# Optimization experiments

Hardware: AMD Instinct MI355X
Metric: run time of the kernel (lower is better)

## Reference

```python
import jax, jax.numpy as jnp
import numpy as np

N_NODES = 50000
N_EDGES = 800000
IN_FEAT = 512
OUT_FEAT = 128


def multispike(x):
    return jnp.floor(jnp.clip(4.0 * x, 0.0, 4.0) + 0.5) / 4.0


def setup_inputs() -> dict:
    key = jax.random.key(0)
    k1, k2, k3, k4, k5 = jax.random.split(key, 5)
    feat = jax.random.normal(k1, (N_NODES, IN_FEAT), dtype=jnp.float32)
    # Xavier-uniform-like init for the weight parameter
    limit = np.sqrt(6.0 / (IN_FEAT + OUT_FEAT)).astype(np.float32)
    weight = jax.random.uniform(k2, (IN_FEAT, OUT_FEAT), dtype=jnp.float32,
                                minval=-limit, maxval=limit)
    rows = jnp.sort(jax.random.randint(k3, (N_EDGES,), 0, N_NODES, dtype=jnp.int32))
    cols = jax.random.randint(k4, (N_EDGES,), 0, N_NODES, dtype=jnp.int32)
    edge_weight = jax.random.uniform(k5, (N_EDGES,), dtype=jnp.float32)
    return {"feat": feat, "weight": weight, "rows": rows, "cols": cols,
            "edge_weight": edge_weight}


def reference(feat, weight, rows, cols, edge_weight):
    # x = feat @ W                     [N, out_feat]
    x = jnp.matmul(feat, weight)
    # x = spmm(adj, x): out[i] = sum_{e: rows[e]==i} w_e * x[cols[e]]
    edge_feats = edge_weight[:, None] * x[cols]          # [E, out_feat]
    x = jax.ops.segment_sum(edge_feats, rows, num_segments=N_NODES)
    # quantized multi-spike activation
    return multispike(x)
```

## Files before the change

### kernel.cpp

```cpp
#include <hip/hip_runtime.h>

#define N_NODES 50000
#define N_EDGES 800000
#define IN_FEAT 512
#define OUT_FEAT 128

#define GEMM_BLOCKS ((N_NODES + 31) / 32)
#define ROWPTR_BLOCKS ((N_NODES + 1 + 63) / 64)


__device__ __forceinline__ float multispike(float a) {
    return floorf(fminf(fmaxf(4.0f * a, 0.0f), 4.0f) + 0.5f) * 0.25f;
}

__device__ __forceinline__ int bswz(int q) { return q ^ ((q >> 3) & 1); }

__global__ __launch_bounds__(64) void gemm_rowptr_kernel(
    const float* __restrict__ A, const float* __restrict__ B,
    float* __restrict__ C, int M,
    const int* __restrict__ rows, int* __restrict__ row_ptr) {
    __shared__ float As[32][36];
    __shared__ float Bs[32][128];

    const int tid = threadIdx.x;

    if (blockIdx.x >= GEMM_BLOCKS) {
        int i = (blockIdx.x - GEMM_BLOCKS) * 64 + tid;
        if (i <= N_NODES) {
            int lo = 0, hi = N_EDGES;
            while (lo < hi) {
                int mid = (lo + hi) >> 1;
                if (rows[mid] < i) lo = mid + 1; else hi = mid;
            }
            row_ptr[i] = lo;
        }
        return;
    }

    const int tx = tid & 15;
    const int ty = tid >> 4;
    const int block_m = blockIdx.x * 32;

    const int bq0 = bswz(2 * tx) * 4;
    const int bq1 = bswz(2 * tx + 1) * 4;

    float acc[8][8];
#pragma unroll
    for (int i = 0; i < 8; i++)
#pragma unroll
        for (int j = 0; j < 8; j++) acc[i][j] = 0.0f;

    for (int k0 = 0; k0 < IN_FEAT; k0 += 32) {
#pragma unroll
        for (int i = 0; i < 4; i++) {
            int f = tid + i * 64;
            int r = f >> 3;
            int kq = (f & 7) << 2;
            int gm = block_m + r;
            float4 v = make_float4(0.f, 0.f, 0.f, 0.f);
            if (gm < M) v = *(const float4*)(A + (size_t)gm * IN_FEAT + k0 + kq);
            As[kq + 0][r] = v.x;
            As[kq + 1][r] = v.y;
            As[kq + 2][r] = v.z;
            As[kq + 3][r] = v.w;
        }
#pragma unroll
        for (int i = 0; i < 16; i++) {
            int f = tid + i * 64;
            int r = f >> 5;
            int q = f & 31;
            *(float4*)&Bs[r][bswz(q) * 4] =
                *(const float4*)(B + (size_t)(k0 + r) * OUT_FEAT + q * 4);
        }
        __syncthreads();

#pragma unroll
        for (int k = 0; k < 32; k++) {
            float4 a0 = *(const float4*)&As[k][ty * 8];
            float4 a1 = *(const float4*)&As[k][ty * 8 + 4];
            float4 b0 = *(const float4*)&Bs[k][bq0];
            float4 b1 = *(const float4*)&Bs[k][bq1];
            float av[8] = {a0.x, a0.y, a0.z, a0.w, a1.x, a1.y, a1.z, a1.w};
            float bv[8] = {b0.x, b0.y, b0.z, b0.w, b1.x, b1.y, b1.z, b1.w};
#pragma unroll
            for (int i = 0; i < 8; i++)
#pragma unroll
                for (int j = 0; j < 8; j++)
                    acc[i][j] = fmaf(av[i], bv[j], acc[i][j]);
        }
        __syncthreads();
    }

#pragma unroll
    for (int i = 0; i < 8; i++) {
        int gm = block_m + ty * 8 + i;
        if (gm < M) {
            float* cp = C + (size_t)gm * OUT_FEAT + tx * 8;
            *(float4*)cp = make_float4(acc[i][0], acc[i][1], acc[i][2], acc[i][3]);
            *(float4*)(cp + 4) = make_float4(acc[i][4], acc[i][5], acc[i][6], acc[i][7]);
        }
    }
}

__global__ __launch_bounds__(256) void spmm_kernel(const float* __restrict__ x,
                                                   const int* __restrict__ cols,
                                                   const float* __restrict__ ew,
                                                   const int* __restrict__ row_ptr,
                                                   float* __restrict__ out) {
    const int wave = threadIdx.x >> 6;
    const int lane = threadIdx.x & 63;
    const int r = blockIdx.x * 4 + wave;
    if (r >= N_NODES) return;

    const int e0 = row_ptr[r];
    const int e1 = row_ptr[r + 1];
    const int niter = (e1 - e0 + 15) >> 4;
    const float2* __restrict__ x2 = (const float2*)x;

    float accx = 0.0f, accy = 0.0f;

    for (int t = 0; t < niter; t++) {
        const int base = e0 + t * 16;
        int c[16];
        float w[16];
#pragma unroll
        for (int j = 0; j < 16; j++) {
            int e = base + j;
            int ee = (e < e1) ? e : (e1 - 1);
            c[j] = cols[ee];
            w[j] = (e < e1) ? ew[ee] : 0.0f;
        }
        float2 v[16];
#pragma unroll
        for (int j = 0; j < 16; j++) {
            v[j] = x2[(size_t)c[j] * 64 + lane];
        }
#pragma unroll
        for (int j = 0; j < 16; j++) {
            accx = fmaf(w[j], v[j].x, accx);
            accy = fmaf(w[j], v[j].y, accy);
        }
    }

    float2* out2 = (float2*)out;
    out2[(size_t)r * 64 + lane] = make_float2(multispike(accx), multispike(accy));
}

extern "C" void kernel_launch(void* const* d_in, const int* in_sizes, int n_in,
                              void* d_out, int out_size, void* d_ws, size_t ws_size,
                              hipStream_t stream) {
    const float* feat = (const float*)d_in[0];
    const float* weight = (const float*)d_in[1];
    const int* rows = (const int*)d_in[2];
    const int* cols = (const int*)d_in[3];
    const float* ew = (const float*)d_in[4];
    float* out = (float*)d_out;

    float* x = (float*)d_ws;
    int* row_ptr = (int*)((char*)d_ws + (size_t)N_NODES * OUT_FEAT * sizeof(float));

    gemm_rowptr_kernel<<<GEMM_BLOCKS + ROWPTR_BLOCKS, 64, 0, stream>>>(
        feat, weight, x, N_NODES, rows, row_ptr);
    spmm_kernel<<<(N_NODES + 3) / 4, 256, 0, stream>>>(x, cols, ew, row_ptr, out);
}
```

Measured before the change: 364.8 us.

## Replace shared-memory GEMM tiles with register-streamed A rows and wave-uniform B loads

The GEMM drops the LDS-tiled 32x128 block scheme. Each lane now owns one output row and each wave owns 8 output columns, with the column offset made wave-uniform through readfirstlane so B can be read with scalar loads. A rows are kept in registers and prefetched one k-chunk ahead, which removes the __syncthreads barriers and shared-memory traffic. In exchange each thread accumulates only 8 outputs, so arithmetic intensity per thread is lower, and A is re-read once per N-half and relies on cache. Blocks grow to 512 threads and the row_ptr part is remapped to match.

```diff
diff --git a/kernel.cpp b/kernel.cpp
--- a/kernel.cpp
+++ b/kernel.cpp
@@ -5,27 +5,23 @@
 #define IN_FEAT 512
 #define OUT_FEAT 128
 
-#define GEMM_BLOCKS ((N_NODES + 31) / 32)
-#define ROWPTR_BLOCKS ((N_NODES + 1 + 63) / 64)
+#define M_STRIPES ((N_NODES + 63) / 64)
+#define GEMM_BLOCKS (M_STRIPES * 2)
+#define ROWPTR_BLOCKS ((N_NODES + 1 + 511) / 512)
 
 
 __device__ __forceinline__ float multispike(float a) {
     return floorf(fminf(fmaxf(4.0f * a, 0.0f), 4.0f) + 0.5f) * 0.25f;
 }
 
-__device__ __forceinline__ int bswz(int q) { return q ^ ((q >> 3) & 1); }
-
-__global__ __launch_bounds__(64) void gemm_rowptr_kernel(
+__global__ __launch_bounds__(512, 4) void gemm_rowptr_kernel(
     const float* __restrict__ A, const float* __restrict__ B,
     float* __restrict__ C, int M,
     const int* __restrict__ rows, int* __restrict__ row_ptr) {
-    __shared__ float As[32][36];
-    __shared__ float Bs[32][128];
-
     const int tid = threadIdx.x;
 
     if (blockIdx.x >= GEMM_BLOCKS) {
-        int i = (blockIdx.x - GEMM_BLOCKS) * 64 + tid;
+        int i = (blockIdx.x - GEMM_BLOCKS) * 512 + tid;
         if (i <= N_NODES) {
             int lo = 0, hi = N_EDGES;
             while (lo < hi) {
@@ -37,68 +33,57 @@
         return;
     }
 
-    const int tx = tid & 15;
-    const int ty = tid >> 4;
-    const int block_m = blockIdx.x * 32;
+    const int stripe = blockIdx.x >> 1;
+    const int n_half = blockIdx.x & 1;
+    const int wave = tid >> 6;
+    const int lane = tid & 63;
 
-    const int bq0 = bswz(2 * tx) * 4;
-    const int bq1 = bswz(2 * tx + 1) * 4;
+    const int n0 = __builtin_amdgcn_readfirstlane(n_half * 64 + wave * 8);
+    const float* __restrict__ Bu = B + n0;
 
-    float acc[8][8];
+    const int gm = stripe * 64 + lane;
+    const float* __restrict__ Arow =
+        A + (size_t)(gm < M ? gm : M - 1) * IN_FEAT;
+
+    float acc[8];
 #pragma unroll
-    for (int i = 0; i < 8; i++)
+    for (int j = 0; j < 8; j++) acc[j] = 0.0f;
+
+    float4 a_cur[8];
 #pragma unroll
-        for (int j = 0; j < 8; j++) acc[i][j] = 0.0f;
+    for (int i = 0; i < 8; i++) a_cur[i] = *(const float4*)(Arow + i * 4);
 
-    for (int k0 = 0; k0 < IN_FEAT; k0 += 32) {
+#pragma unroll 2
+    for (int t = 0; t < 16; t++) {
+        const int k0 = t * 32;
+        float4 a_nxt[8];
+        if (t < 15) {
 #pragma unroll
-        for (int i = 0; i < 4; i++) {
-            int f = tid + i * 64;
-            int r = f >> 3;
-            int kq = (f & 7) << 2;
-            int gm = block_m + r;
-            float4 v = make_float4(0.f, 0.f, 0.f, 0.f);
-            if (gm < M) v = *(const float4*)(A + (size_t)gm * IN_FEAT + k0 + kq);
-            As[kq + 0][r] = v.x;
-            As[kq + 1][r] = v.y;
-            As[kq + 2][r] = v.z;
-            As[kq + 3][r] = v.w;
+            for (int i = 0; i < 8; i++)
+                a_nxt[i] = *(const float4*)(Arow + k0 + 32 + i * 4);
+        }
+
+#pragma unroll
+        for (int kq = 0; kq < 8; kq++) {
+            const float4 av = a_cur[kq];
+#pragma unroll
+            for (int kk = 0; kk < 4; kk++) {
+                const float a = (kk == 0) ? av.x : (kk == 1) ? av.y
+                              : (kk == 2) ? av.z : av.w;
+                const float* bp = Bu + (size_t)(k0 + kq * 4 + kk) * OUT_FEAT;
+#pragma unroll
+                for (int j = 0; j < 8; j++)
+                    acc[j] = fmaf(bp[j], a, acc[j]);
+            }
         }
 #pragma unroll
-        for (int i = 0; i < 16; i++) {
-            int f = tid + i * 64;
-            int r = f >> 5;
-            int q = f & 31;
-            *(float4*)&Bs[r][bswz(q) * 4] =
-                *(const float4*)(B + (size_t)(k0 + r) * OUT_FEAT + q * 4);
-        }
-        __syncthreads();
-
-#pragma unroll
-        for (int k = 0; k < 32; k++) {
-            float4 a0 = *(const float4*)&As[k][ty * 8];
-            float4 a1 = *(const float4*)&As[k][ty * 8 + 4];
-            float4 b0 = *(const float4*)&Bs[k][bq0];
-            float4 b1 = *(const float4*)&Bs[k][bq1];
-            float av[8] = {a0.x, a0.y, a0.z, a0.w, a1.x, a1.y, a1.z, a1.w};
-            float bv[8] = {b0.x, b0.y, b0.z, b0.w, b1.x, b1.y, b1.z, b1.w};
-#pragma unroll
-            for (int i = 0; i < 8; i++)
-#pragma unroll
-                for (int j = 0; j < 8; j++)
-                    acc[i][j] = fmaf(av[i], bv[j], acc[i][j]);
-        }
-        __syncthreads();
+        for (int i = 0; i < 8; i++) a_cur[i] = a_nxt[i];
     }
 
-#pragma unroll
-    for (int i = 0; i < 8; i++) {
-        int gm = block_m + ty * 8 + i;
-        if (gm < M) {
-            float* cp = C + (size_t)gm * OUT_FEAT + tx * 8;
-            *(float4*)cp = make_float4(acc[i][0], acc[i][1], acc[i][2], acc[i][3]);
-            *(float4*)(cp + 4) = make_float4(acc[i][4], acc[i][5], acc[i][6], acc[i][7]);
-        }
+    if (gm < M) {
+        float* cp = C + (size_t)gm * OUT_FEAT + n0;
+        *(float4*)cp = make_float4(acc[0], acc[1], acc[2], acc[3]);
+        *(float4*)(cp + 4) = make_float4(acc[4], acc[5], acc[6], acc[7]);
     }
 }
 
@@ -159,7 +144,7 @@
     float* x = (float*)d_ws;
     int* row_ptr = (int*)((char*)d_ws + (size_t)N_NODES * OUT_FEAT * sizeof(float));
 
-    gemm_rowptr_kernel<<<GEMM_BLOCKS + ROWPTR_BLOCKS, 64, 0, stream>>>(
+    gemm_rowptr_kernel<<<GEMM_BLOCKS + ROWPTR_BLOCKS, 512, 0, stream>>>(
         feat, weight, x, N_NODES, rows, row_ptr);
     spmm_kernel<<<(N_NODES + 3) / 4, 256, 0, stream>>>(x, cols, ew, row_ptr, out);
 }
```

After: 485.8 us. 33.2% more time.
